# Performance work log

Measured on AMD Instinct MI355X. Metric: run time of the kernel, lower is better.

The kernel has to match this reference:

```python
import jax, jax.numpy as jnp
import numpy as np
import math

B, S, D = 16, 577, 768          # batch, seq (24*24 grid + 1 cls), in_dim=att_dim
H, HD = 12, 64                  # heads, head_dim
GRID = 24                       # height = width; S = GRID*GRID + rpe_skip
RATIO = 1.9
ALPHA, BETA, GAMMA = 1.0 * RATIO, 2.0 * RATIO, 8.0 * RATIO
BETA_INT = int(BETA)            # 3
NUM_BUCKETS = (2 * BETA_INT + 1) ** 2 + 1  # 49 product buckets + 1 extra for skip (cls) = 50


def _piecewise_index(d):
    # iRPE piecewise bucket index (numpy, static). d: integer offsets.
    d = d.astype(np.float64)
    ad = np.abs(d)
    log_part = ALPHA + np.log(np.maximum(ad, 1e-9) / ALPHA) / math.log(GAMMA / ALPHA) * (BETA - ALPHA)
    y_out = np.sign(d) * np.clip(np.round(log_part), None, BETA)
    idx = np.where(ad <= ALPHA, np.round(d), y_out)
    return np.trunc(idx).astype(np.int64)  # torch .to(int) truncates toward zero


def make_rp_bucket():
    # 2D 'product' method bucket ids with skip=1 (cls token -> extra bucket)
    ii, jj = np.meshgrid(np.arange(GRID), np.arange(GRID), indexing='ij')
    pos = np.stack([ii.ravel(), jj.ravel()], axis=-1)          # (L,2)
    diff = pos[:, None, :] - pos[None, :, :]                    # (L,L,2)
    Sb = 2 * BETA_INT + 1
    r = _piecewise_index(diff[..., 0]) + BETA_INT               # [0, 2*beta_int]
    c = _piecewise_index(diff[..., 1]) + BETA_INT
    pid = r * Sb + c                                            # [0, 48]
    L = GRID * GRID
    bucket = np.full((L + 1, L + 1), NUM_BUCKETS - 1, dtype=np.int32)
    bucket[1:, 1:] = pid
    return jnp.asarray(bucket)


def setup_inputs() -> dict:
    key = jax.random.key(0)
    k1, k2, k3 = jax.random.split(key, 3)
    x = jax.random.normal(k1, (B, S, D), dtype=jnp.float32)
    w_qkv = jax.random.normal(k2, (3 * D, D), dtype=jnp.float32) * 0.02   # torch Linear weight (out,in)
    rpe_table = jax.random.normal(k3, (HD, NUM_BUCKETS), dtype=jnp.float32) * 0.02  # shared-head contextual table
    rp_bucket = make_rp_bucket()                                # (S,S) int32
    return {"x": x, "w_qkv": w_qkv, "rpe_table": rpe_table, "rp_bucket": rp_bucket}


def reference(x, w_qkv, rpe_table, rp_bucket):
    qkv = x @ w_qkv.T                                           # (B,S,3D)
    q, k, v = jnp.split(qkv, 3, axis=-1)
    # Faithful to torch source: plain reshape (B,S,D)->(B,H,S,HD) (no transpose-split)
    scale = 1.0 / jnp.sqrt(jnp.asarray(HD, x.dtype))
    q = q.reshape(B, H, S, HD) * scale
    k = k.reshape(B, H, S, HD)
    v = v.reshape(B, H, S, HD)
    qk = jnp.einsum('bhid,bhjd->bhij', q, k)                    # (B,H,S,S)
    # contextual rpe_k: bias[b,h,i,j] = (q[b,h,i] . rpe_table[:, rp_bucket[i,j]])
    ctx = jnp.einsum('bhid,dc->bhic', q, rpe_table)             # (B,H,S,NUM_BUCKETS)
    idx = jnp.broadcast_to(rp_bucket[None, None].astype(jnp.int32), (B, H, S, S))
    bias = jnp.take_along_axis(ctx, idx, axis=-1)               # (B,H,S,S)
    att = jax.nn.softmax(qk + bias, axis=-1)
    out = jnp.einsum('bhij,bhjd->bhid', att, v)                 # (B,H,S,HD)
    y = out.transpose(0, 2, 1, 3).reshape(B, S, D)              # out_proj is Identity (out_dim==att_dim)
    return y
```

## Files before the change

### kernel.cpp

```cpp
#include <hip/hip_runtime.h>

constexpr int BN_  = 16;
constexpr int SN_  = 577;
constexpr int SP_  = 640;
constexpr int DN_  = 768;
constexpr int HN_  = 12;
constexpr int HD_  = 64;
constexpr int NB_  = 50;
constexpr int MR_  = BN_ * SN_;
constexpr int MRP_ = 73 * 128;
constexpr int NQ_  = 3 * DN_;
constexpr int BHS_ = BN_ * HN_ * SN_;
constexpr int SHD_ = SN_ * HD_;

typedef __attribute__((ext_vector_type(8))) short short8;
typedef __attribute__((ext_vector_type(4))) float f32x4;

__device__ __forceinline__ short f2bf(float f) {
  union { float f; unsigned u; } v; v.f = f;
  unsigned r = (v.u + 0x7fffu + ((v.u >> 16) & 1u)) >> 16;
  return (short)r;
}

__device__ __forceinline__ float ex2(float x) {
  float r; asm("v_exp_f32 %0, %1" : "=v"(r) : "v"(x)); return r;
}

__launch_bounds__(256)
__global__ void cvt_k(const float* __restrict__ src, short* __restrict__ dst,
                      int n_src, int n_dst) {
  const int i = (blockIdx.x * 256 + threadIdx.x) * 8;
  if (i >= n_dst) return;
  union { short8 v; short u[8]; } pk;
  if (i < n_src) {
    const float4 a = *(const float4*)(src + i);
    const float4 b = *(const float4*)(src + i + 4);
    pk.u[0] = f2bf(a.x); pk.u[1] = f2bf(a.y); pk.u[2] = f2bf(a.z); pk.u[3] = f2bf(a.w);
    pk.u[4] = f2bf(b.x); pk.u[5] = f2bf(b.y); pk.u[6] = f2bf(b.z); pk.u[7] = f2bf(b.w);
  } else {
#pragma unroll
    for (int j = 0; j < 8; ++j) pk.u[j] = 0;
  }
  *(short8*)(dst + i) = pk.v;
}

__launch_bounds__(256)
__global__ void rpb8_k(const int* __restrict__ rpb, unsigned char* __restrict__ rpbu8) {
  const int tid = blockIdx.x * 256 + threadIdx.x;
  if (tid >= SN_ * 160) return;
  const int i = tid / 160, c4 = tid - i * 160;
  const int j = c4 * 4;
  uchar4 o;
  o.x = (j     < SN_) ? (unsigned char)rpb[i * SN_ + j    ] : 0;
  o.y = (j + 1 < SN_) ? (unsigned char)rpb[i * SN_ + j + 1] : 0;
  o.z = (j + 2 < SN_) ? (unsigned char)rpb[i * SN_ + j + 2] : 0;
  o.w = (j + 3 < SN_) ? (unsigned char)rpb[i * SN_ + j + 3] : 0;
  *(uchar4*)(rpbu8 + (size_t)i * 640 + j) = o;
}

__launch_bounds__(256)
__global__ void qkv_mfma_k(const short* __restrict__ xb, const short* __restrict__ wb,
                           short* __restrict__ Qbf, short* __restrict__ Ksw,
                           short* __restrict__ Vbf) {
  __shared__ short At[128 * 64];
  __shared__ short Bt[128 * 64];
  const int t = threadIdx.x;
  const int w = t >> 6, lane = t & 63, g = lane >> 4, ln = lane & 15;
  const int wm = w >> 1, wn = w & 1;
  const int m0 = blockIdx.y * 128, n0 = blockIdx.x * 128;

  const int sr = t >> 1, su = (t & 1) * 4;
  const short* ga = xb + (size_t)(m0 + sr) * DN_ + su * 8;
  const short* gb = wb + (size_t)(n0 + sr) * DN_ + su * 8;
  short* la = At + sr * 64;
  short* lb = Bt + sr * 64;
  const int swr = sr & 7;

  f32x4 acc[4][4];
#pragma unroll
  for (int mt = 0; mt < 4; ++mt)
#pragma unroll
    for (int nt = 0; nt < 4; ++nt) acc[mt][nt] = (f32x4){0.f, 0.f, 0.f, 0.f};

  short8 ra[4], rb[4];
#pragma unroll
  for (int u = 0; u < 4; ++u) {
    ra[u] = *(const short8*)(ga + u * 8);
    rb[u] = *(const short8*)(gb + u * 8);
  }

  for (int k0 = 0; k0 < DN_; k0 += 64) {
    __syncthreads();
#pragma unroll
    for (int u = 0; u < 4; ++u) {
      *(short8*)(la + (((su + u) ^ swr) * 8)) = ra[u];
      *(short8*)(lb + (((su + u) ^ swr) * 8)) = rb[u];
    }
    __syncthreads();
    if (k0 + 64 < DN_) {
#pragma unroll
      for (int u = 0; u < 4; ++u) {
        ra[u] = *(const short8*)(ga + k0 + 64 + u * 8);
        rb[u] = *(const short8*)(gb + k0 + 64 + u * 8);
      }
    }
#pragma unroll
    for (int kc = 0; kc < 2; ++kc) {
      short8 af[4], bf[4];
#pragma unroll
      for (int mt = 0; mt < 4; ++mt) {
        const int row = wm * 64 + mt * 16 + ln;
        const int u = (kc * 4 + g) ^ (row & 7);
        af[mt] = *(const short8*)&At[row * 64 + u * 8];
      }
#pragma unroll
      for (int nt = 0; nt < 4; ++nt) {
        const int row = wn * 64 + nt * 16 + ln;
        const int u = (kc * 4 + g) ^ (row & 7);
        bf[nt] = *(const short8*)&Bt[row * 64 + u * 8];
      }
#pragma unroll
      for (int mt = 0; mt < 4; ++mt)
#pragma unroll
        for (int nt = 0; nt < 4; ++nt)
          acc[mt][nt] = __builtin_amdgcn_mfma_f32_16x16x32_bf16(af[mt], bf[nt], acc[mt][nt], 0, 0, 0);
    }
  }

  const int nw0  = n0 + wn * 64;
  const int secg = nw0 / DN_;
  const int cbw  = nw0 - secg * DN_;
  const float QSC = 0.18033688011112042f;
#pragma unroll
  for (int mt = 0; mt < 4; ++mt) {
#pragma unroll
    for (int r = 0; r < 4; ++r) {
      const int gm = m0 + wm * 64 + mt * 16 + 4 * g + r;
      if (gm >= MR_) continue;
      const int bb = gm / SN_;
      const int ss = gm - bb * SN_;
      const int pb = ss * DN_ + cbw;
#pragma unroll
      for (int nt = 0; nt < 4; ++nt) {
        const int p   = pb + nt * 16 + ln;
        const int hh  = p / SHD_;
        const int rem = p - hh * SHD_;
        const int ii  = rem >> 6;
        const int dd  = rem & 63;
        const size_t ro = (size_t)(bb * HN_ + hh);
        const float v = acc[mt][nt][r];
        if (secg == 0) {
          Qbf[(ro * SN_ + ii) * 64 + dd] = f2bf(v * QSC);
        } else if (secg == 1) {
          Ksw[(ro * SP_ + ii) * 64 + (dd ^ ((ii & 7) << 3))] = f2bf(v);
        } else {
          Vbf[(ro * SP_ + ii) * 64 + dd] = f2bf(v);
        }
      }
    }
  }
}

__launch_bounds__(256)
__global__ void vtr_k(const short* __restrict__ Vbf, short* __restrict__ Vtsw) {
  __shared__ short T[64][72];
  const int t = threadIdx.x;
  const int jt = blockIdx.x, bh = blockIdx.y;
  const int j0 = jt * 64;
  {
    const int r = t >> 2, c0 = (t & 3) * 16;
    const short* src = Vbf + ((size_t)bh * SP_ + j0 + r) * 64 + c0;
    *(short8*)&T[r][c0]     = *(const short8*)(src);
    *(short8*)&T[r][c0 + 8] = *(const short8*)(src + 8);
  }
  __syncthreads();
  const int d = t >> 2;
  short* dst = Vtsw + ((size_t)bh * 64 + d) * SP_;
  const int sw = (d & 7) << 3;
#pragma unroll
  for (int e = 0; e < 4; ++e) {
    const int jl = (t & 3) * 16 + e * 4;
    const int jg = j0 + jl;
    short4 v;
    v.x = (jg + 0 < SN_) ? T[jl + 0][d] : (short)0;
    v.y = (jg + 1 < SN_) ? T[jl + 1][d] : (short)0;
    v.z = (jg + 2 < SN_) ? T[jl + 2][d] : (short)0;
    v.w = (jg + 3 < SN_) ? T[jl + 3][d] : (short)0;
    *(short4*)&dst[jg ^ sw] = v;
  }
}

__launch_bounds__(256)
__global__ void attn_k(const short* __restrict__ Qbf, const short* __restrict__ Ksw,
                       const short* __restrict__ Vtsw, const float* __restrict__ rpe,
                       const unsigned char* __restrict__ rpbu8, float* __restrict__ y) {
  __shared__ short Kt[64 * 64];
  __shared__ short Vt[64 * 64];
  __shared__ float ctxs[4][16][53];
  __shared__ char urp[8192];
  short (*Rp)[64] = (short (*)[64])urp;
  unsigned char* rpbt = (unsigned char*)urp;

  const int t = threadIdx.x;
  const int w = t >> 6, lane = t & 63, g = lane >> 4, ln = lane & 15;
  const int qt = blockIdx.x, bh = blockIdx.y;
  const int b = bh / HN_, h = bh - b * HN_;
  const int i0 = qt * 64;
  const size_t rb = (size_t)bh * SN_;
  const short* Kbh = Ksw + (size_t)bh * SP_ * 64;
  const short* Vbh = Vtsw + (size_t)bh * 64 * SP_;

  const int sr_ = t >> 2, scu_ = (t & 3) * 16;
  const int irow_s = (i0 + sr_ <= SN_ - 1) ? (i0 + sr_) : (SN_ - 1);

  short8 kr0, kr1, vr0, vr1; int4 rp_;
  {
    const short* ks = Kbh + (size_t)sr_ * 64 + scu_;
    kr0 = *(const short8*)(ks); kr1 = *(const short8*)(ks + 8);
    const short* vs = Vbh + (size_t)sr_ * SP_ + scu_;
    vr0 = *(const short8*)(vs); vr1 = *(const short8*)(vs + 8);
    rp_ = *(const int4*)(rpbu8 + (size_t)irow_s * 640 + scu_);
  }

  for (int e = t; e < 64 * 64; e += 256) {
    const int c = e >> 6, d = e & 63;
    Rp[c][d] = (c < NB_) ? f2bf(rpe[d * NB_ + c]) : (short)0;
  }

  short8 qf[2];
  {
    int row = i0 + 16 * w + ln; if (row > SN_ - 1) row = SN_ - 1;
    const short* qp = Qbf + (rb + row) * 64;
    qf[0] = *(const short8*)(qp + 8 * g);
    qf[1] = *(const short8*)(qp + 32 + 8 * g);
  }

  __syncthreads();

  {
    f32x4 accC[4];
#pragma unroll
    for (int ct = 0; ct < 4; ++ct) accC[ct] = (f32x4){0.f, 0.f, 0.f, 0.f};
#pragma unroll
    for (int kc = 0; kc < 2; ++kc) {
#pragma unroll
      for (int ct = 0; ct < 4; ++ct) {
        const short8 rf = *(const short8*)&Rp[ct * 16 + ln][kc * 32 + 8 * g];
        accC[ct] = __builtin_amdgcn_mfma_f32_16x16x32_bf16(qf[kc], rf, accC[ct], 0, 0, 0);
      }
    }
#pragma unroll
    for (int ct = 0; ct < 4; ++ct) {
      const int c = ct * 16 + ln;
      if (c < 53) {
#pragma unroll
        for (int r = 0; r < 4; ++r) ctxs[w][4 * g + r][c] = accC[ct][r];
      }
    }
  }

  float m = -3e38f, l = 0.f;
  f32x4 accO[4];
#pragma unroll
  for (int dt = 0; dt < 4; ++dt) accO[dt] = (f32x4){0.f, 0.f, 0.f, 0.f};

  const int swv = (ln & 7) << 3;
  const float* cbase = &ctxs[w][ln][0];
  const int rpoff = (16 * w + ln) * 80;

  for (int jt = 0; jt < 10; ++jt) {
    const int j0 = jt * 64;
    __syncthreads();
    *(short8*)&Kt[sr_ * 64 + scu_]     = kr0;
    *(short8*)&Kt[sr_ * 64 + scu_ + 8] = kr1;
    *(short8*)&Vt[sr_ * 64 + scu_]     = vr0;
    *(short8*)&Vt[sr_ * 64 + scu_ + 8] = vr1;
    *(int4*)&rpbt[sr_ * 80 + scu_]     = rp_;
    __syncthreads();

    if (jt < 9) {
      const int jn = j0 + 64;
      const short* ks = Kbh + (size_t)(jn + sr_) * 64 + scu_;
      kr0 = *(const short8*)(ks); kr1 = *(const short8*)(ks + 8);
      const short* vs = Vbh + (size_t)sr_ * SP_ + jn + scu_;
      vr0 = *(const short8*)(vs); vr1 = *(const short8*)(vs + 8);
      rp_ = *(const int4*)(rpbu8 + (size_t)irow_s * 640 + jn + scu_);
    }

    f32x4 accS[4];
#pragma unroll
    for (int nt = 0; nt < 4; ++nt) accS[nt] = (f32x4){0.f, 0.f, 0.f, 0.f};
#pragma unroll
    for (int kc = 0; kc < 2; ++kc) {
      const int cb = (kc * 32 + 8 * g) ^ swv;
#pragma unroll
      for (int nt = 0; nt < 4; ++nt) {
        const short8 kf = *(const short8*)&Kt[(nt * 16 + ln) * 64 + cb];
        accS[nt] = __builtin_amdgcn_mfma_f32_16x16x32_bf16(kf, qf[kc], accS[nt], 0, 0, 0);
      }
    }

    float pv[4][4];
#pragma unroll
    for (int nt = 0; nt < 4; ++nt) {
      const uchar4 bk = *(const uchar4*)&rpbt[rpoff + nt * 16 + 4 * g];
      pv[nt][0] = accS[nt][0] + cbase[bk.x];
      pv[nt][1] = accS[nt][1] + cbase[bk.y];
      pv[nt][2] = accS[nt][2] + cbase[bk.z];
      pv[nt][3] = accS[nt][3] + cbase[bk.w];
    }
    if (jt == 9) {
#pragma unroll
      for (int nt = 0; nt < 4; ++nt) {
        const int jb = j0 + nt * 16 + 4 * g;
#pragma unroll
        for (int r = 0; r < 4; ++r)
          if (jb + r >= SN_) pv[nt][r] = -3e38f;
      }
    }

    float mx = fmaxf(fmaxf(pv[0][0], pv[0][1]), fmaxf(pv[0][2], pv[0][3]));
#pragma unroll
    for (int nt = 1; nt < 4; ++nt)
      mx = fmaxf(mx, fmaxf(fmaxf(pv[nt][0], pv[nt][1]), fmaxf(pv[nt][2], pv[nt][3])));
    mx = fmaxf(mx, __shfl_xor(mx, 16));
    mx = fmaxf(mx, __shfl_xor(mx, 32));

    if (__any(mx > m + 8.f)) {
      const float mnew = fmaxf(m, mx);
      const float sc = ex2(m - mnew);
      float scr[4];
#pragma unroll
      for (int r = 0; r < 4; ++r) scr[r] = __shfl(sc, 4 * g + r);
#pragma unroll
      for (int dt = 0; dt < 4; ++dt)
#pragma unroll
        for (int r = 0; r < 4; ++r) accO[dt][r] *= scr[r];
      l *= sc;
      m = mnew;
    }

    float sum = 0.f;
#pragma unroll
    for (int nt = 0; nt < 4; ++nt)
#pragma unroll
      for (int r = 0; r < 4; ++r) {
        const float p = ex2(pv[nt][r] - m);
        pv[nt][r] = p;
        sum += p;
      }
    sum += __shfl_xor(sum, 16);
    sum += __shfl_xor(sum, 32);
    l += sum;

    short8 pf[2];
#pragma unroll
    for (int kc = 0; kc < 2; ++kc) {
      union { short8 v; short u[8]; } pk;
#pragma unroll
      for (int r = 0; r < 4; ++r) {
        pk.u[r]     = f2bf(pv[2 * kc][r]);
        pk.u[4 + r] = f2bf(pv[2 * kc + 1][r]);
      }
      pf[kc] = pk.v;
    }

#pragma unroll
    for (int kc = 0; kc < 2; ++kc) {
#pragma unroll
      for (int dt = 0; dt < 4; ++dt) {
        const short* vrow = &Vt[(dt * 16 + ln) * 64];
        union { short8 v; short4 hh[2]; } u;
        u.hh[0] = *(const short4*)&vrow[(kc * 32 + 4 * g) ^ swv];
        u.hh[1] = *(const short4*)&vrow[(kc * 32 + 16 + 4 * g) ^ swv];
        accO[dt] = __builtin_amdgcn_mfma_f32_16x16x32_bf16(pf[kc], u.v, accO[dt], 0, 0, 0);
      }
    }
  }

  float linv[4];
#pragma unroll
  for (int r = 0; r < 4; ++r) linv[r] = 1.f / __shfl(l, 4 * g + r);
#pragma unroll
  for (int r = 0; r < 4; ++r) {
    const int i = i0 + 16 * w + 4 * g + r;
    if (i >= SN_) continue;
    float* yp = y + ((size_t)b * SN_ + i) * DN_ + h * HD_ + ln;
#pragma unroll
    for (int dt = 0; dt < 4; ++dt) yp[dt * 16] = accO[dt][r] * linv[r];
  }
}

extern "C" void kernel_launch(void* const* d_in, const int* in_sizes, int n_in,
                              void* d_out, int out_size, void* d_ws, size_t ws_size,
                              hipStream_t stream) {
  const float* x   = (const float*)d_in[0];
  const float* w   = (const float*)d_in[1];
  const float* rpe = (const float*)d_in[2];
  const int*   rpb = (const int*)d_in[3];
  float* y = (float*)d_out;

  short* xb   = (short*)d_ws;
  short* wb   = xb + (size_t)MRP_ * DN_;
  short* Qbf  = wb + (size_t)NQ_ * DN_;
  short* Ksw  = Qbf + (size_t)BHS_ * HD_;
  short* Vbf  = Ksw + (size_t)BN_ * HN_ * SP_ * 64;
  short* Vtsw = Vbf + (size_t)BN_ * HN_ * SP_ * 64;
  unsigned char* rpbu8 = (unsigned char*)(Vtsw + (size_t)BN_ * HN_ * 64 * SP_);

  cvt_k<<<dim3(MRP_ * DN_ / 2048), 256, 0, stream>>>(x, xb, MR_ * DN_, MRP_ * DN_);
  cvt_k<<<dim3(NQ_ * DN_ / 2048), 256, 0, stream>>>(w, wb, NQ_ * DN_, NQ_ * DN_);
  rpb8_k<<<dim3((SN_ * 160 + 255) / 256), 256, 0, stream>>>(rpb, rpbu8);
  qkv_mfma_k<<<dim3(18, 73), 256, 0, stream>>>(xb, wb, Qbf, Ksw, Vbf);
  vtr_k<<<dim3(10, BN_ * HN_), 256, 0, stream>>>(Vbf, Vtsw);
  attn_k<<<dim3(10, BN_ * HN_), 256, 0, stream>>>(Qbf, Ksw, Vtsw, rpe, rpbu8, y);
}
```

Baseline: 160.4 us.

## Remap attention grid for XCD locality, bf16 ctx, packed cvt, MFMA priority

The attention kernel now launches on a 1D grid and remaps block ids so that all query tiles of one batch-head land on the same XCD, which should improve L2 reuse of K/V. The contextual bias table in shared memory is stored as bf16 instead of fp32, halving its LDS footprint at some cost in precision. The P-matrix conversion to bf16 uses the hardware packed v_cvt_pk_bf16_f32 instruction instead of the manual rounding. s_setprio raises wave priority around the MFMA blocks to help interleave matrix work with the softmax of other waves.

```diff
diff --git a/kernel.cpp b/kernel.cpp
--- a/kernel.cpp
+++ b/kernel.cpp
@@ -24,6 +24,15 @@
 
 __device__ __forceinline__ float ex2(float x) {
   float r; asm("v_exp_f32 %0, %1" : "=v"(r) : "v"(x)); return r;
+}
+
+__device__ __forceinline__ unsigned cvtpk(float a, float b) {
+  unsigned r; asm("v_cvt_pk_bf16_f32 %0, %1, %2" : "=v"(r) : "v"(a), "v"(b));
+  return r;
+}
+
+__device__ __forceinline__ float bf2f(unsigned short u) {
+  union { unsigned u; float f; } v; v.u = ((unsigned)u) << 16; return v.f;
 }
 
 __launch_bounds__(256)
@@ -196,14 +205,17 @@
                        const unsigned char* __restrict__ rpbu8, float* __restrict__ y) {
   __shared__ short Kt[64 * 64];
   __shared__ short Vt[64 * 64];
-  __shared__ float ctxs[4][16][53];
+  __shared__ unsigned short ctxs[4][16][53];
   __shared__ char urp[8192];
   short (*Rp)[64] = (short (*)[64])urp;
   unsigned char* rpbt = (unsigned char*)urp;
 
   const int t = threadIdx.x;
   const int w = t >> 6, lane = t & 63, g = lane >> 4, ln = lane & 15;
-  const int qt = blockIdx.x, bh = blockIdx.y;
+  const int wg = blockIdx.x;
+  const int xcd = wg & 7, idx = wg >> 3;
+  const int qt = idx % 10;
+  const int bh = (idx / 10) * 8 + xcd;
   const int b = bh / HN_, h = bh - b * HN_;
   const int i0 = qt * 64;
   const size_t rb = (size_t)bh * SN_;
@@ -254,7 +266,8 @@
       const int c = ct * 16 + ln;
       if (c < 53) {
 #pragma unroll
-        for (int r = 0; r < 4; ++r) ctxs[w][4 * g + r][c] = accC[ct][r];
+        for (int r = 0; r < 4; ++r)
+          ctxs[w][4 * g + r][c] = (unsigned short)f2bf(accC[ct][r]);
       }
     }
   }
@@ -265,7 +278,7 @@
   for (int dt = 0; dt < 4; ++dt) accO[dt] = (f32x4){0.f, 0.f, 0.f, 0.f};
 
   const int swv = (ln & 7) << 3;
-  const float* cbase = &ctxs[w][ln][0];
+  const unsigned short* cbase = &ctxs[w][ln][0];
   const int rpoff = (16 * w + ln) * 80;
 
   for (int jt = 0; jt < 10; ++jt) {
@@ -290,6 +303,7 @@
     f32x4 accS[4];
 #pragma unroll
     for (int nt = 0; nt < 4; ++nt) accS[nt] = (f32x4){0.f, 0.f, 0.f, 0.f};
+    __builtin_amdgcn_s_setprio(1);
 #pragma unroll
     for (int kc = 0; kc < 2; ++kc) {
       const int cb = (kc * 32 + 8 * g) ^ swv;
@@ -299,15 +313,16 @@
         accS[nt] = __builtin_amdgcn_mfma_f32_16x16x32_bf16(kf, qf[kc], accS[nt], 0, 0, 0);
       }
     }
+    __builtin_amdgcn_s_setprio(0);
 
     float pv[4][4];
 #pragma unroll
     for (int nt = 0; nt < 4; ++nt) {
       const uchar4 bk = *(const uchar4*)&rpbt[rpoff + nt * 16 + 4 * g];
-      pv[nt][0] = accS[nt][0] + cbase[bk.x];
-      pv[nt][1] = accS[nt][1] + cbase[bk.y];
-      pv[nt][2] = accS[nt][2] + cbase[bk.z];
-      pv[nt][3] = accS[nt][3] + cbase[bk.w];
+      pv[nt][0] = accS[nt][0] + bf2f(cbase[bk.x]);
+      pv[nt][1] = accS[nt][1] + bf2f(cbase[bk.y]);
+      pv[nt][2] = accS[nt][2] + bf2f(cbase[bk.z]);
+      pv[nt][3] = accS[nt][3] + bf2f(cbase[bk.w]);
     }
     if (jt == 9) {
 #pragma unroll
@@ -356,15 +371,15 @@
     short8 pf[2];
 #pragma unroll
     for (int kc = 0; kc < 2; ++kc) {
-      union { short8 v; short u[8]; } pk;
-#pragma unroll
-      for (int r = 0; r < 4; ++r) {
-        pk.u[r]     = f2bf(pv[2 * kc][r]);
-        pk.u[4 + r] = f2bf(pv[2 * kc + 1][r]);
-      }
+      union { short8 v; unsigned wd[4]; } pk;
+      pk.wd[0] = cvtpk(pv[2 * kc][0],     pv[2 * kc][1]);
+      pk.wd[1] = cvtpk(pv[2 * kc][2],     pv[2 * kc][3]);
+      pk.wd[2] = cvtpk(pv[2 * kc + 1][0], pv[2 * kc + 1][1]);
+      pk.wd[3] = cvtpk(pv[2 * kc + 1][2], pv[2 * kc + 1][3]);
       pf[kc] = pk.v;
     }
 
+    __builtin_amdgcn_s_setprio(1);
 #pragma unroll
     for (int kc = 0; kc < 2; ++kc) {
 #pragma unroll
@@ -376,6 +391,7 @@
         accO[dt] = __builtin_amdgcn_mfma_f32_16x16x32_bf16(pf[kc], u.v, accO[dt], 0, 0, 0);
       }
     }
+    __builtin_amdgcn_s_setprio(0);
   }
 
   float linv[4];
@@ -413,5 +429,5 @@
   rpb8_k<<<dim3((SN_ * 160 + 255) / 256), 256, 0, stream>>>(rpb, rpbu8);
   qkv_mfma_k<<<dim3(18, 73), 256, 0, stream>>>(xb, wb, Qbf, Ksw, Vbf);
   vtr_k<<<dim3(10, BN_ * HN_), 256, 0, stream>>>(Vbf, Vtsw);
-  attn_k<<<dim3(10, BN_ * HN_), 256, 0, stream>>>(Qbf, Ksw, Vtsw, rpe, rpbu8, y);
-}
+  attn_k<<<dim3(1920), 256, 0, stream>>>(Qbf, Ksw, Vtsw, rpe, rpbu8, y);
+}
```

New measurement: 159.4 us. About the same (-0.6%).
